# Optimization experiments

Hardware: AMD Instinct MI355X
Metric: run time of the kernel (lower is better)

Reference implementation:

```python
import jax, jax.numpy as jnp
import numpy as np

NEG = -1e9


def setup_inputs() -> dict:
    key = jax.random.key(0)
    ks = jax.random.split(key, 10)
    B, C, H, W = 4, 64, 64, 64
    Cq = C // 8
    x = jax.random.normal(ks[0], (B, C, H, W), dtype=jnp.float32)
    mask = jax.random.randint(ks[1], (B, 1, H, W), 0, 2, dtype=jnp.int32)
    # 1x1 conv params (out_ch, in_ch) + bias
    Wq = jax.random.normal(ks[2], (Cq, C), dtype=jnp.float32) * (1.0 / np.sqrt(C))
    bq = jnp.zeros((Cq,), dtype=jnp.float32)
    Wk = jax.random.normal(ks[3], (Cq, C), dtype=jnp.float32) * (1.0 / np.sqrt(C))
    bk = jnp.zeros((Cq,), dtype=jnp.float32)
    Wv = jax.random.normal(ks[4], (C, C), dtype=jnp.float32) * (1.0 / np.sqrt(C))
    bv = jnp.zeros((C,), dtype=jnp.float32)
    # torch inits gamma to 0; use small random so attention path contributes
    gamma = jax.random.normal(ks[5], (1,), dtype=jnp.float32) * 0.1
    return {"x": x, "mask": mask, "Wq": Wq, "bq": bq, "Wk": Wk, "bk": bk,
            "Wv": Wv, "bv": bv, "gamma": gamma}


def reference(x, mask, Wq, bq, Wk, bk, Wv, bv, gamma):
    B, C, H, W = x.shape
    N = H * W
    xf = x.reshape(B, C, N)                      # (B,C,N)
    # 1x1 convs == per-pixel linear projections
    q = jnp.einsum('oc,bcn->bno', Wq, xf) + bq   # (B,N,Cq)
    k = jnp.einsum('oc,bcn->bon', Wk, xf) + bk[None, :, None]  # (B,Cq,N)
    v = jnp.einsum('oc,bcn->bon', Wv, xf) + bv[None, :, None]  # (B,C,N)
    m = mask.reshape(B, N).astype(bool)
    logits = jnp.einsum('bno,bom->bnm', q, k)    # (B,N,N)
    valid = m[:, :, None] & m[:, None, :]        # outer-product validity mask
    logits = jnp.where(valid, logits, NEG)
    attn = jax.nn.softmax(logits, axis=-1)       # (B,N,N)
    out = jnp.einsum('bcj,bij->bci', v, attn)    # (B,C,N)
    out = out.reshape(B, C, H, W)
    return gamma * out + x
```

## Files before the change

### kernel.cpp

```cpp
#include <hip/hip_runtime.h>

typedef unsigned int uint;
typedef unsigned short ushort;
typedef __attribute__((ext_vector_type(8))) short short8;
typedef __attribute__((ext_vector_type(4))) float f32x4;
typedef __attribute__((ext_vector_type(16))) float f32x16;
typedef __attribute__((ext_vector_type(4))) uint uint4v;
typedef __attribute__((ext_vector_type(2))) uint uint2v;

#define BATCH 4
#define CH 64
#define NPIX 4096
#define LOG2E 1.44269504f

#define WSQ 0
#define WSK (BATCH * 128 * 512)
#define WSV (2 * BATCH * 128 * 512)

__device__ __forceinline__ ushort f2bf(float f) {
    union { float f; uint u; } a; a.f = f;
    const uint u = a.u;
    return (ushort)((u + 0x7FFFu + ((u >> 16) & 1u)) >> 16);
}
__device__ __forceinline__ uint pkbf(float a, float b) {
    return (uint)f2bf(a) | ((uint)f2bf(b) << 16);
}
__device__ __forceinline__ uint pkbf_fu(float a, float b) {
    union { float f; uint u; } x, y; x.f = a; y.f = b;
    return ((y.u + 0x8000u) & 0xFFFF0000u) | ((x.u + 0x8000u) >> 16);
}

__global__ __launch_bounds__(256) void proj_kernel(
    const float* __restrict__ x, const int* __restrict__ mask,
    const float* __restrict__ Wq, const float* __restrict__ bq,
    const float* __restrict__ Wk, const float* __restrict__ bk,
    const float* __restrict__ Wv, const float* __restrict__ bv,
    ushort* __restrict__ ws)
{
    __shared__ float wsh[16 * 64];
    __shared__ float bsh[16];
    const int g = blockIdx.y;
    const int tid = threadIdx.x;
    const int nout = (g == 0) ? 16 : 8;

    if (g == 0) {
        for (int i = tid; i < 512; i += 256) { wsh[i] = Wq[i]; wsh[512 + i] = Wk[i]; }
        if (tid < 8)  bsh[tid] = bq[tid];
        else if (tid < 16) bsh[tid] = bk[tid - 8];
    } else {
        const float* W = Wv + (g - 1) * 512;
        for (int i = tid; i < 512; i += 256) wsh[i] = W[i];
        if (tid < 8) bsh[tid] = bv[(g - 1) * 8 + tid];
    }
    __syncthreads();

    const int pix = blockIdx.x * 256 + tid;
    const int b = pix >> 12;
    const int n = pix & (NPIX - 1);
    const float* xb = x + (size_t)b * CH * NPIX + n;

    float acc[16];
#pragma unroll
    for (int o = 0; o < 16; o++) acc[o] = (o < nout) ? bsh[o] : 0.f;

#pragma unroll
    for (int c4 = 0; c4 < 16; c4++) {
        float xv0 = xb[(size_t)(c4 * 4 + 0) * NPIX];
        float xv1 = xb[(size_t)(c4 * 4 + 1) * NPIX];
        float xv2 = xb[(size_t)(c4 * 4 + 2) * NPIX];
        float xv3 = xb[(size_t)(c4 * 4 + 3) * NPIX];
        if (g == 0) {
#pragma unroll
            for (int o = 0; o < 16; o++) {
                const int base = (o < 8 ? 0 : 512) + (o & 7) * 64;
                float4 w = *(const float4*)&wsh[base + c4 * 4];
                acc[o] += w.x * xv0 + w.y * xv1 + w.z * xv2 + w.w * xv3;
            }
        } else {
#pragma unroll
            for (int o = 0; o < 8; o++) {
                float4 w = *(const float4*)&wsh[o * 64 + c4 * 4];
                acc[o] += w.x * xv0 + w.y * xv1 + w.z * xv2 + w.w * xv3;
            }
        }
    }

    const int jt = n >> 5, jl = n & 31;
    if (g == 0) {
        const int qm = mask[pix];
        {
            const float s = qm ? LOG2E : 0.f;
            uint4v lo, hi;
            lo.x = pkbf(acc[0] * s, acc[1] * s);
            lo.y = pkbf(acc[2] * s, acc[3] * s);
            lo.z = pkbf(acc[4] * s, acc[5] * s);
            lo.w = pkbf(acc[6] * s, acc[7] * s);
            hi.x = qm ? 0x3F80u : 0u;
            hi.y = 0u; hi.z = 0u; hi.w = 0u;
            ushort* qf = ws + WSQ + (size_t)b * 65536 + (size_t)jt * 512;
            *(uint4v*)(qf + jl * 8)       = lo;
            *(uint4v*)(qf + 256 + jl * 8) = hi;
        }
        {
            uint4v lo, hi;
            lo.x = pkbf(acc[8],  acc[9]);
            lo.y = pkbf(acc[10], acc[11]);
            lo.z = pkbf(acc[12], acc[13]);
            lo.w = pkbf(acc[14], acc[15]);
            hi.x = (uint)f2bf(qm ? 0.f : -1e30f);
            hi.y = 0u; hi.z = 0u; hi.w = 0u;
            ushort* kf = ws + WSK + (size_t)b * 65536 + (size_t)jt * 512;
            *(uint4v*)(kf + jl * 8)       = lo;
            *(uint4v*)(kf + 256 + jl * 8) = hi;
        }
    } else {
        const int h = jl >> 4, hp = (jl >> 3) & 1, jj = jl & 7;
        const int c0 = (g - 1) * 8;
        ushort* vt = ws + WSV + (size_t)b * 262144;
#pragma unroll
        for (int o = 0; o < 8; o++) {
            const int c = c0 + o, ct = c >> 5, cp = c & 31;
            vt[(size_t)((((jt * 2 + ct) * 2 + h) * 2 + hp) * 256) + cp * 8 + jj] = f2bf(acc[o]);
        }
    }
}

__global__ __launch_bounds__(512, 2) void attn_kernel(
    const ushort* __restrict__ ws, const float* __restrict__ x,
    const float* __restrict__ gamma, float* __restrict__ out)
{
    __shared__ float Obuf[8][32][36];
    __shared__ float Lb[2][8][32];
    __shared__ float Linv[2][32];

    const int tid  = threadIdx.x;
    const int wid  = tid >> 6;
    const int lane = tid & 63;
    const int hl   = lane >> 5;
    const int col  = lane & 31;
    const int b    = blockIdx.y;
    const int bx   = blockIdx.x;

    const ushort* qf = ws + WSQ + (size_t)b * 65536 + (size_t)(2 * bx) * 512;
    const ushort* kf = ws + WSK + (size_t)b * 65536;
    const ushort* vt = ws + WSV + (size_t)b * 262144;

    const short8 qfA = *(const short8*)(qf + lane * 8);
    const short8 qfB = *(const short8*)(qf + 512 + lane * 8);

    f32x16 accA0, accA1, accB0, accB1, zf;
#pragma unroll
    for (int r = 0; r < 16; r++) { accA0[r] = 0.f; accA1[r] = 0.f; accB0[r] = 0.f; accB1[r] = 0.f; zf[r] = 0.f; }
    float lsA = 0.f, lsB = 0.f;

    int jt = wid;
    uint4v kn   = *(const uint4v*)(kf + (size_t)jt * 512 + lane * 8);
    uint4v vn00 = *(const uint4v*)(vt + (size_t)((jt * 2 + 0) * 2 + 0) * 512 + lane * 8);
    uint4v vn01 = *(const uint4v*)(vt + (size_t)((jt * 2 + 0) * 2 + 1) * 512 + lane * 8);
    uint4v vn10 = *(const uint4v*)(vt + (size_t)((jt * 2 + 1) * 2 + 0) * 512 + lane * 8);
    uint4v vn11 = *(const uint4v*)(vt + (size_t)((jt * 2 + 1) * 2 + 1) * 512 + lane * 8);

#define QK_PV(SFRAG, LSUM, A0, A1) do {                                                              \
    float p[16];                                                                                     \
    _Pragma("unroll") for (int r = 0; r < 16; r++) p[r] = __builtin_amdgcn_exp2f((SFRAG)[r]);        \
    LSUM += (((p[0] + p[1]) + (p[2] + p[3])) + ((p[4] + p[5]) + (p[6] + p[7])))                      \
          + (((p[8] + p[9]) + (p[10] + p[11])) + ((p[12] + p[13]) + (p[14] + p[15])));               \
    uint P[8];                                                                                       \
    _Pragma("unroll") for (int r = 0; r < 8; r++) P[r] = pkbf_fu(p[2 * r], p[2 * r + 1]);            \
    const uint2v s02 = __builtin_amdgcn_permlane32_swap(P[0], P[2], false, false);                   \
    const uint2v s13 = __builtin_amdgcn_permlane32_swap(P[1], P[3], false, false);                   \
    const uint2v s46 = __builtin_amdgcn_permlane32_swap(P[4], P[6], false, false);                   \
    const uint2v s57 = __builtin_amdgcn_permlane32_swap(P[5], P[7], false, false);                   \
    uint4v B0, B1;                                                                                   \
    B0.x = s02.x; B0.y = s13.x; B0.z = s02.y; B0.w = s13.y;                                          \
    B1.x = s46.x; B1.y = s57.x; B1.z = s46.y; B1.w = s57.y;                                          \
    __builtin_amdgcn_s_setprio(1);                                                                   \
    A0 = __builtin_amdgcn_mfma_f32_32x32x16_bf16(*(const short8*)&c00, *(const short8*)&B0, A0, 0, 0, 0); \
    A0 = __builtin_amdgcn_mfma_f32_32x32x16_bf16(*(const short8*)&c01, *(const short8*)&B1, A0, 0, 0, 0); \
    A1 = __builtin_amdgcn_mfma_f32_32x32x16_bf16(*(const short8*)&c10, *(const short8*)&B0, A1, 0, 0, 0); \
    A1 = __builtin_amdgcn_mfma_f32_32x32x16_bf16(*(const short8*)&c11, *(const short8*)&B1, A1, 0, 0, 0); \
    __builtin_amdgcn_s_setprio(0);                                                                   \
} while (0)

    for (int t = 0; t < 16; t++) {
        const uint4v kc = kn, c00 = vn00, c01 = vn01, c10 = vn10, c11 = vn11;
        if (t < 15) {
            const int jn = jt + 8;
            kn   = *(const uint4v*)(kf + (size_t)jn * 512 + lane * 8);
            vn00 = *(const uint4v*)(vt + (size_t)((jn * 2 + 0) * 2 + 0) * 512 + lane * 8);
            vn01 = *(const uint4v*)(vt + (size_t)((jn * 2 + 0) * 2 + 1) * 512 + lane * 8);
            vn10 = *(const uint4v*)(vt + (size_t)((jn * 2 + 1) * 2 + 0) * 512 + lane * 8);
            vn11 = *(const uint4v*)(vt + (size_t)((jn * 2 + 1) * 2 + 1) * 512 + lane * 8);
        }

        const f32x16 sA = __builtin_amdgcn_mfma_f32_32x32x16_bf16(*(const short8*)&kc, qfA, zf, 0, 0, 0);
        const f32x16 sB = __builtin_amdgcn_mfma_f32_32x32x16_bf16(*(const short8*)&kc, qfB, zf, 0, 0, 0);

        QK_PV(sA, lsA, accA0, accA1);
        QK_PV(sB, lsB, accB0, accB1);

        jt += 8;
    }
#undef QK_PV

    const float lwA = lsA + __shfl_xor(lsA, 32);
    const float lwB = lsB + __shfl_xor(lsB, 32);
    if (hl == 0) { Lb[0][wid][col] = lwA; Lb[1][wid][col] = lwB; }
    __syncthreads();
    if (tid < 64) {
        const int q = tid >> 5, m = tid & 31;
        float s = 0.f;
#pragma unroll
        for (int w = 0; w < 8; w++) s += Lb[q][w][m];
        Linv[q][m] = 1.f / s;
    }

    const float gm = gamma[0];

#define MERGE_PASS(ACC, QSEL, CHALF) do {                                                            \
    __syncthreads();                                                                                 \
    _Pragma("unroll") for (int r = 0; r < 16; r++) {                                                 \
        const int crow = (r & 3) + 8 * (r >> 2) + 4 * hl;            \
        Obuf[wid][crow][col] = (ACC)[r];                                                             \
    }                                                                                                \
    __syncthreads();                                                                                 \
    {                                                                                                \
        const int c = tid >> 4, m0 = (tid & 15) * 2;                                                 \
        float o0 = 0.f, o1 = 0.f;                                                                    \
        _Pragma("unroll") for (int w = 0; w < 8; w++) { o0 += Obuf[w][c][m0]; o1 += Obuf[w][c][m0 + 1]; } \
        const size_t base = (((size_t)(b * CH + (CHALF) * 32 + c)) << 12) + bx * 64 + (QSEL) * 32 + m0; \
        const float2 xv = *(const float2*)&x[base];                                                  \
        float2 rv;                                                                                   \
        rv.x = gm * o0 * Linv[QSEL][m0]     + xv.x;                                                  \
        rv.y = gm * o1 * Linv[QSEL][m0 + 1] + xv.y;                                                  \
        *(float2*)&out[base] = rv;                                                                   \
    }                                                                                                \
} while (0)

    MERGE_PASS(accA0, 0, 0);
    MERGE_PASS(accA1, 0, 1);
    MERGE_PASS(accB0, 1, 0);
    MERGE_PASS(accB1, 1, 1);
#undef MERGE_PASS
}

extern "C" void kernel_launch(void* const* d_in, const int* in_sizes, int n_in,
                              void* d_out, int out_size, void* d_ws, size_t ws_size,
                              hipStream_t stream) {
    const float* x     = (const float*)d_in[0];
    const int*   mask  = (const int*)d_in[1];
    const float* Wq    = (const float*)d_in[2];
    const float* bq    = (const float*)d_in[3];
    const float* Wk    = (const float*)d_in[4];
    const float* bk    = (const float*)d_in[5];
    const float* Wv    = (const float*)d_in[6];
    const float* bv    = (const float*)d_in[7];
    const float* gamma = (const float*)d_in[8];
    float* out  = (float*)d_out;
    ushort* ws  = (ushort*)d_ws;

    proj_kernel<<<dim3(64, 9), 256, 0, stream>>>(x, mask, Wq, bq, Wk, bk, Wv, bv, ws);
    attn_kernel<<<dim3(64, 4), 512, 0, stream>>>(ws, x, gamma, out);
}
```

Baseline: 100.2 us.

## Compute softmax row sums via MFMA, use hardware bf16 pack, merge output passes

Moves the softmax denominator accumulation off the vector ALU by running extra MFMAs against a one-hot ones operand on the same bf16 P fragments. The software bf16 rounding is replaced with the v_cvt_pk_bf16_f32 instruction in both kernels. The epilogue is restructured to merge both channel halves per query block in one LDS pass with 128-bit loads and stores, halving the barrier rounds at the cost of doubling the LDS buffer. The row sums now come from bf16-rounded probabilities, which slightly changes numerics, and the extra MFMAs add matrix-unit work.

Measured after the change: 100.7 us. Within noise of the previous version (+0.5%).

```diff
diff --git a/kernel.cpp b/kernel.cpp
--- a/kernel.cpp
+++ b/kernel.cpp
@@ -22,12 +22,10 @@
     const uint u = a.u;
     return (ushort)((u + 0x7FFFu + ((u >> 16) & 1u)) >> 16);
 }
-__device__ __forceinline__ uint pkbf(float a, float b) {
-    return (uint)f2bf(a) | ((uint)f2bf(b) << 16);
-}
-__device__ __forceinline__ uint pkbf_fu(float a, float b) {
-    union { float f; uint u; } x, y; x.f = a; y.f = b;
-    return ((y.u + 0x8000u) & 0xFFFF0000u) | ((x.u + 0x8000u) >> 16);
+__device__ __forceinline__ uint cvtpk(float a, float b) {
+    uint r;
+    asm("v_cvt_pk_bf16_f32 %0, %1, %2" : "=v"(r) : "v"(a), "v"(b));
+    return r;
 }
 
 __global__ __launch_bounds__(256) void proj_kernel(
@@ -91,10 +89,10 @@
         {
             const float s = qm ? LOG2E : 0.f;
             uint4v lo, hi;
-            lo.x = pkbf(acc[0] * s, acc[1] * s);
-            lo.y = pkbf(acc[2] * s, acc[3] * s);
-            lo.z = pkbf(acc[4] * s, acc[5] * s);
-            lo.w = pkbf(acc[6] * s, acc[7] * s);
+            lo.x = cvtpk(acc[0] * s, acc[1] * s);
+            lo.y = cvtpk(acc[2] * s, acc[3] * s);
+            lo.z = cvtpk(acc[4] * s, acc[5] * s);
+            lo.w = cvtpk(acc[6] * s, acc[7] * s);
             hi.x = qm ? 0x3F80u : 0u;
             hi.y = 0u; hi.z = 0u; hi.w = 0u;
             ushort* qf = ws + WSQ + (size_t)b * 65536 + (size_t)jt * 512;
@@ -103,10 +101,10 @@
         }
         {
             uint4v lo, hi;
-            lo.x = pkbf(acc[8],  acc[9]);
-            lo.y = pkbf(acc[10], acc[11]);
-            lo.z = pkbf(acc[12], acc[13]);
-            lo.w = pkbf(acc[14], acc[15]);
+            lo.x = cvtpk(acc[8],  acc[9]);
+            lo.y = cvtpk(acc[10], acc[11]);
+            lo.z = cvtpk(acc[12], acc[13]);
+            lo.w = cvtpk(acc[14], acc[15]);
             hi.x = (uint)f2bf(qm ? 0.f : -1e30f);
             hi.y = 0u; hi.z = 0u; hi.w = 0u;
             ushort* kf = ws + WSK + (size_t)b * 65536 + (size_t)jt * 512;
@@ -129,7 +127,7 @@
     const ushort* __restrict__ ws, const float* __restrict__ x,
     const float* __restrict__ gamma, float* __restrict__ out)
 {
-    __shared__ float Obuf[8][32][36];
+    __shared__ float Obuf[8][64][36];
     __shared__ float Lb[2][8][32];
     __shared__ float Linv[2][32];
 
@@ -148,10 +146,19 @@
     const short8 qfA = *(const short8*)(qf + lane * 8);
     const short8 qfB = *(const short8*)(qf + 512 + lane * 8);
 
-    f32x16 accA0, accA1, accB0, accB1, zf;
-#pragma unroll
-    for (int r = 0; r < 16; r++) { accA0[r] = 0.f; accA1[r] = 0.f; accB0[r] = 0.f; accB1[r] = 0.f; zf[r] = 0.f; }
-    float lsA = 0.f, lsB = 0.f;
+    const uint ob = 0x3F803F80u;
+    uint4v oAv, oBv;
+    oAv.x = (col == 0) ? ob : 0u; oAv.y = oAv.x; oAv.z = oAv.x; oAv.w = oAv.x;
+    oBv.x = (col == 1) ? ob : 0u; oBv.y = oBv.x; oBv.z = oBv.x; oBv.w = oBv.x;
+    const short8 onesA = *(const short8*)&oAv;
+    const short8 onesB = *(const short8*)&oBv;
+
+    f32x16 accA0, accA1, accB0, accB1, accL, zf;
+#pragma unroll
+    for (int r = 0; r < 16; r++) {
+        accA0[r] = 0.f; accA1[r] = 0.f; accB0[r] = 0.f; accB1[r] = 0.f;
+        accL[r] = 0.f; zf[r] = 0.f;
+    }
 
     int jt = wid;
     uint4v kn   = *(const uint4v*)(kf + (size_t)jt * 512 + lane * 8);
@@ -160,13 +167,11 @@
     uint4v vn10 = *(const uint4v*)(vt + (size_t)((jt * 2 + 1) * 2 + 0) * 512 + lane * 8);
     uint4v vn11 = *(const uint4v*)(vt + (size_t)((jt * 2 + 1) * 2 + 1) * 512 + lane * 8);
 
-#define QK_PV(SFRAG, LSUM, A0, A1) do {                                                              \
+#define QK_PV(SFRAG, ONES, A0, A1) do {                                                              \
     float p[16];                                                                                     \
     _Pragma("unroll") for (int r = 0; r < 16; r++) p[r] = __builtin_amdgcn_exp2f((SFRAG)[r]);        \
-    LSUM += (((p[0] + p[1]) + (p[2] + p[3])) + ((p[4] + p[5]) + (p[6] + p[7])))                      \
-          + (((p[8] + p[9]) + (p[10] + p[11])) + ((p[12] + p[13]) + (p[14] + p[15])));               \
     uint P[8];                                                                                       \
-    _Pragma("unroll") for (int r = 0; r < 8; r++) P[r] = pkbf_fu(p[2 * r], p[2 * r + 1]);            \
+    _Pragma("unroll") for (int r = 0; r < 8; r++) P[r] = cvtpk(p[2 * r], p[2 * r + 1]);              \
     const uint2v s02 = __builtin_amdgcn_permlane32_swap(P[0], P[2], false, false);                   \
     const uint2v s13 = __builtin_amdgcn_permlane32_swap(P[1], P[3], false, false);                   \
     const uint2v s46 = __builtin_amdgcn_permlane32_swap(P[4], P[6], false, false);                   \
@@ -179,6 +184,8 @@
     A0 = __builtin_amdgcn_mfma_f32_32x32x16_bf16(*(const short8*)&c01, *(const short8*)&B1, A0, 0, 0, 0); \
     A1 = __builtin_amdgcn_mfma_f32_32x32x16_bf16(*(const short8*)&c10, *(const short8*)&B0, A1, 0, 0, 0); \
     A1 = __builtin_amdgcn_mfma_f32_32x32x16_bf16(*(const short8*)&c11, *(const short8*)&B1, A1, 0, 0, 0); \
+    accL = __builtin_amdgcn_mfma_f32_32x32x16_bf16(ONES, *(const short8*)&B0, accL, 0, 0, 0);        \
+    accL = __builtin_amdgcn_mfma_f32_32x32x16_bf16(ONES, *(const short8*)&B1, accL, 0, 0, 0);        \
     __builtin_amdgcn_s_setprio(0);                                                                   \
 } while (0)
 
@@ -196,16 +203,14 @@
         const f32x16 sA = __builtin_amdgcn_mfma_f32_32x32x16_bf16(*(const short8*)&kc, qfA, zf, 0, 0, 0);
         const f32x16 sB = __builtin_amdgcn_mfma_f32_32x32x16_bf16(*(const short8*)&kc, qfB, zf, 0, 0, 0);
 
-        QK_PV(sA, lsA, accA0, accA1);
-        QK_PV(sB, lsB, accB0, accB1);
+        QK_PV(sA, onesA, accA0, accA1);
+        QK_PV(sB, onesB, accB0, accB1);
 
         jt += 8;
     }
 #undef QK_PV
 
-    const float lwA = lsA + __shfl_xor(lsA, 32);
-    const float lwB = lsB + __shfl_xor(lsB, 32);
-    if (hl == 0) { Lb[0][wid][col] = lwA; Lb[1][wid][col] = lwB; }
+    if (hl == 0) { Lb[0][wid][col] = accL[0]; Lb[1][wid][col] = accL[1]; }
     __syncthreads();
     if (tid < 64) {
         const int q = tid >> 5, m = tid & 31;
@@ -217,30 +222,29 @@
 
     const float gm = gamma[0];
 
-#define MERGE_PASS(ACC, QSEL, CHALF) do {                                                            \
+#define MERGE_PASS(A0v, A1v, QSEL) do {                                                              \
     __syncthreads();                                                                                 \
     _Pragma("unroll") for (int r = 0; r < 16; r++) {                                                 \
         const int crow = (r & 3) + 8 * (r >> 2) + 4 * hl;            \
-        Obuf[wid][crow][col] = (ACC)[r];                                                             \
+        Obuf[wid][crow][col]      = (A0v)[r];                                                        \
+        Obuf[wid][32 + crow][col] = (A1v)[r];                                                        \
     }                                                                                                \
     __syncthreads();                                                                                 \
     {                                                                                                \
-        const int c = tid >> 4, m0 = (tid & 15) * 2;                                                 \
-        float o0 = 0.f, o1 = 0.f;                                                                    \
-        _Pragma("unroll") for (int w = 0; w < 8; w++) { o0 += Obuf[w][c][m0]; o1 += Obuf[w][c][m0 + 1]; } \
-        const size_t base = (((size_t)(b * CH + (CHALF) * 32 + c)) << 12) + bx * 64 + (QSEL) * 32 + m0; \
-        const float2 xv = *(const float2*)&x[base];                                                  \
-        float2 rv;                                                                                   \
-        rv.x = gm * o0 * Linv[QSEL][m0]     + xv.x;                                                  \
-        rv.y = gm * o1 * Linv[QSEL][m0 + 1] + xv.y;                                                  \
-        *(float2*)&out[base] = rv;                                                                   \
+        const int c = tid >> 3, m0 = (tid & 7) * 4;                                                  \
+        f32x4 o = {0.f, 0.f, 0.f, 0.f};                                                              \
+        _Pragma("unroll") for (int w = 0; w < 8; w++) o += *(const f32x4*)&Obuf[w][c][m0];            \
+        const size_t base = (((size_t)(b * CH + c)) << 12) + bx * 64 + (QSEL) * 32 + m0;             \
+        const f32x4 xv = *(const f32x4*)&x[base];                                                    \
+        f32x4 rv;                                                                                    \
+        _Pragma("unroll") for (int u = 0; u < 4; u++)                                                \
+            rv[u] = gm * o[u] * Linv[QSEL][m0 + u] + xv[u];                                          \
+        *(f32x4*)&out[base] = rv;                                                                    \
     }                                                                                                \
 } while (0)
 
-    MERGE_PASS(accA0, 0, 0);
-    MERGE_PASS(accA1, 0, 1);
-    MERGE_PASS(accB0, 1, 0);
-    MERGE_PASS(accB1, 1, 1);
+    MERGE_PASS(accA0, accA1, 0);
+    MERGE_PASS(accB0, accB1, 1);
 #undef MERGE_PASS
 }
 
```

## Compact valid keys per row group and skip masked key tiles in attention

Applied to the files above, without the earlier changes.

The projection kernel now stream-compacts each 256-pixel group's keys and values so valid (mask=1) keys come first, records per-group valid counts, stores per-pixel query masks, and computes per-channel V sums for the fully masked queries. The attention kernel builds a per-wave list of key tiles that contain valid keys and iterates only over those, skipping tiles that are entirely masked. Masked queries are given the uniform-attention result, the V mean, directly in the epilogue. Bf16 packing also switches to the hardware v_cvt_pk_bf16_f32 instruction. This adds preprocessing, extra workspace traffic and an indirect tile-index table, and it relies on masked keys contributing exp(-inf)=0, which matches the reference's -1e9 fill.

New measurement: 96.47 us. 1.04x faster.

```diff
diff --git a/kernel.cpp b/kernel.cpp
--- a/kernel.cpp
+++ b/kernel.cpp
@@ -2,6 +2,7 @@
 
 typedef unsigned int uint;
 typedef unsigned short ushort;
+typedef unsigned long long ull;
 typedef __attribute__((ext_vector_type(8))) short short8;
 typedef __attribute__((ext_vector_type(4))) float f32x4;
 typedef __attribute__((ext_vector_type(16))) float f32x16;
@@ -14,20 +15,21 @@
 #define LOG2E 1.44269504f
 
 #define WSQ 0
-#define WSK (BATCH * 128 * 512)
-#define WSV (2 * BATCH * 128 * 512)
+#define WSK 262144
+#define WSV 524288
+#define WSNV 1572864
+#define WSQM 1572928
+#define WSVPU 1589312
 
 __device__ __forceinline__ ushort f2bf(float f) {
     union { float f; uint u; } a; a.f = f;
     const uint u = a.u;
     return (ushort)((u + 0x7FFFu + ((u >> 16) & 1u)) >> 16);
 }
-__device__ __forceinline__ uint pkbf(float a, float b) {
-    return (uint)f2bf(a) | ((uint)f2bf(b) << 16);
-}
-__device__ __forceinline__ uint pkbf_fu(float a, float b) {
-    union { float f; uint u; } x, y; x.f = a; y.f = b;
-    return ((y.u + 0x8000u) & 0xFFFF0000u) | ((x.u + 0x8000u) >> 16);
+__device__ __forceinline__ uint cvtpk(float a, float b) {
+    uint r;
+    asm("v_cvt_pk_bf16_f32 %0, %1, %2" : "=v"(r) : "v"(a), "v"(b));
+    return r;
 }
 
 __global__ __launch_bounds__(256) void proj_kernel(
@@ -39,8 +41,11 @@
 {
     __shared__ float wsh[16 * 64];
     __shared__ float bsh[16];
+    __shared__ int   wcnt[4];
+    __shared__ float wvs[4][8];
     const int g = blockIdx.y;
     const int tid = threadIdx.x;
+    const int wid = tid >> 6, lane = tid & 63;
     const int nout = (g == 0) ? 16 : 8;
 
     if (g == 0) {
@@ -52,13 +57,16 @@
         for (int i = tid; i < 512; i += 256) wsh[i] = W[i];
         if (tid < 8) bsh[tid] = bv[(g - 1) * 8 + tid];
     }
-    __syncthreads();
 
     const int pix = blockIdx.x * 256 + tid;
     const int b = pix >> 12;
     const int n = pix & (NPIX - 1);
+    const int qm = mask[pix];
+    const ull bal = __ballot(qm != 0);
+    if (lane == 0) wcnt[wid] = __popcll(bal);
+    __syncthreads();
+
     const float* xb = x + (size_t)b * CH * NPIX + n;
-
     float acc[16];
 #pragma unroll
     for (int o = 0; o < 16; o++) acc[o] = (o < nout) ? bsh[o] : 0.f;
@@ -85,34 +93,48 @@
         }
     }
 
-    const int jt = n >> 5, jl = n & 31;
+    int offV = 0, offI = 0, nvb = 0;
+#pragma unroll
+    for (int w = 0; w < 4; w++) {
+        const int cw = wcnt[w];
+        if (w < wid) { offV += cw; offI += 64 - cw; }
+        nvb += cw;
+    }
+    const int rankV = __popcll(bal & ((1ull << lane) - 1ull));
+    const int slot = qm ? (offV + rankV) : (nvb + offI + (lane - rankV));
+    const int rr = n >> 8;
+    const int js = rr * 8 + (slot >> 5);
+    const int jl = slot & 31;
+
     if (g == 0) {
-        const int qm = mask[pix];
         {
+            const int jtq = n >> 5, jlq = n & 31;
             const float s = qm ? LOG2E : 0.f;
             uint4v lo, hi;
-            lo.x = pkbf(acc[0] * s, acc[1] * s);
-            lo.y = pkbf(acc[2] * s, acc[3] * s);
-            lo.z = pkbf(acc[4] * s, acc[5] * s);
-            lo.w = pkbf(acc[6] * s, acc[7] * s);
+            lo.x = cvtpk(acc[0] * s, acc[1] * s);
+            lo.y = cvtpk(acc[2] * s, acc[3] * s);
+            lo.z = cvtpk(acc[4] * s, acc[5] * s);
+            lo.w = cvtpk(acc[6] * s, acc[7] * s);
             hi.x = qm ? 0x3F80u : 0u;
             hi.y = 0u; hi.z = 0u; hi.w = 0u;
-            ushort* qf = ws + WSQ + (size_t)b * 65536 + (size_t)jt * 512;
-            *(uint4v*)(qf + jl * 8)       = lo;
-            *(uint4v*)(qf + 256 + jl * 8) = hi;
+            ushort* qf = ws + WSQ + (size_t)b * 65536 + (size_t)jtq * 512;
+            *(uint4v*)(qf + jlq * 8)       = lo;
+            *(uint4v*)(qf + 256 + jlq * 8) = hi;
         }
         {
             uint4v lo, hi;
-            lo.x = pkbf(acc[8],  acc[9]);
-            lo.y = pkbf(acc[10], acc[11]);
-            lo.z = pkbf(acc[12], acc[13]);
-            lo.w = pkbf(acc[14], acc[15]);
+            lo.x = cvtpk(acc[8],  acc[9]);
+            lo.y = cvtpk(acc[10], acc[11]);
+            lo.z = cvtpk(acc[12], acc[13]);
+            lo.w = cvtpk(acc[14], acc[15]);
             hi.x = (uint)f2bf(qm ? 0.f : -1e30f);
             hi.y = 0u; hi.z = 0u; hi.w = 0u;
-            ushort* kf = ws + WSK + (size_t)b * 65536 + (size_t)jt * 512;
+            ushort* kf = ws + WSK + (size_t)b * 65536 + (size_t)js * 512;
             *(uint4v*)(kf + jl * 8)       = lo;
             *(uint4v*)(kf + 256 + jl * 8) = hi;
         }
+        if (tid == 0) ws[WSNV + b * 16 + rr] = (ushort)nvb;
+        ws[WSQM + pix] = (ushort)qm;
     } else {
         const int h = jl >> 4, hp = (jl >> 3) & 1, jj = jl & 7;
         const int c0 = (g - 1) * 8;
@@ -120,7 +142,20 @@
 #pragma unroll
         for (int o = 0; o < 8; o++) {
             const int c = c0 + o, ct = c >> 5, cp = c & 31;
-            vt[(size_t)((((jt * 2 + ct) * 2 + h) * 2 + hp) * 256) + cp * 8 + jj] = f2bf(acc[o]);
+            vt[(size_t)((((js * 2 + ct) * 2 + h) * 2 + hp) * 256) + cp * 8 + jj] = f2bf(acc[o]);
+        }
+#pragma unroll
+        for (int o = 0; o < 8; o++) {
+            float v = acc[o];
+#pragma unroll
+            for (int off = 32; off; off >>= 1) v += __shfl_down(v, off);
+            if (lane == 0) wvs[wid][o] = v;
+        }
+        __syncthreads();
+        if (tid < 8) {
+            const float t = wvs[0][tid] + wvs[1][tid] + wvs[2][tid] + wvs[3][tid];
+            float* vpf = (float*)(ws + WSVPU);
+            vpf[(b * 64 + c0 + tid) * 16 + (blockIdx.x & 15)] = t;
         }
     }
 }
@@ -132,6 +167,10 @@
     __shared__ float Obuf[8][32][36];
     __shared__ float Lb[2][8][32];
     __shared__ float Linv[2][32];
+    __shared__ float VmeanS[64];
+    __shared__ ushort qmS[64];
+    __shared__ ushort nvS[16];
+    __shared__ ushort jtT[8][17];
 
     const int tid  = threadIdx.x;
     const int wid  = tid >> 6;
@@ -148,17 +187,51 @@
     const short8 qfA = *(const short8*)(qf + lane * 8);
     const short8 qfB = *(const short8*)(qf + 512 + lane * 8);
 
+    if (tid < 16) nvS[tid] = ws[WSNV + b * 16 + tid];
+    if (tid >= 64 && tid < 128) qmS[tid - 64] = ws[WSQM + b * 4096 + bx * 64 + (tid - 64)];
+    if (tid >= 128 && tid < 192) {
+        const int c = tid - 128;
+        const float* vpf = (const float*)(ws + WSVPU);
+        float s = 0.f;
+#pragma unroll
+        for (int k2 = 0; k2 < 16; k2++) s += vpf[(b * 64 + c) * 16 + k2];
+        VmeanS[c] = s * (1.0f / 4096.0f);
+    }
+    __syncthreads();
+
+    int A = 0;
+#pragma unroll
+    for (int r2 = 0; r2 < 16; r2++) {
+        int a = ((int)nvS[r2] + 31) >> 5; if (a > 8) a = 8;
+        A += a;
+    }
+    if (tid < 128) {
+        const int w = tid >> 4, ii = tid & 15, ci = w + ii * 8;
+        int Acc = 0, ent = 0;
+#pragma unroll
+        for (int r2 = 0; r2 < 16; r2++) {
+            int a = ((int)nvS[r2] + 31) >> 5; if (a > 8) a = 8;
+            if (ci >= Acc && ci < Acc + a) ent = r2 * 8 + (ci - Acc);
+            Acc += a;
+        }
+        jtT[w][ii] = (ushort)ent;
+    }
+    if (tid < 8) jtT[tid][16] = 0;
+    __syncthreads();
+
+    const int niter = (A - wid + 7) >> 3;
+
     f32x16 accA0, accA1, accB0, accB1, zf;
 #pragma unroll
     for (int r = 0; r < 16; r++) { accA0[r] = 0.f; accA1[r] = 0.f; accB0[r] = 0.f; accB1[r] = 0.f; zf[r] = 0.f; }
     float lsA = 0.f, lsB = 0.f;
 
-    int jt = wid;
-    uint4v kn   = *(const uint4v*)(kf + (size_t)jt * 512 + lane * 8);
-    uint4v vn00 = *(const uint4v*)(vt + (size_t)((jt * 2 + 0) * 2 + 0) * 512 + lane * 8);
-    uint4v vn01 = *(const uint4v*)(vt + (size_t)((jt * 2 + 0) * 2 + 1) * 512 + lane * 8);
-    uint4v vn10 = *(const uint4v*)(vt + (size_t)((jt * 2 + 1) * 2 + 0) * 512 + lane * 8);
-    uint4v vn11 = *(const uint4v*)(vt + (size_t)((jt * 2 + 1) * 2 + 1) * 512 + lane * 8);
+    int jc = jtT[wid][0];
+    uint4v kn   = *(const uint4v*)(kf + (size_t)jc * 512 + lane * 8);
+    uint4v vn00 = *(const uint4v*)(vt + (size_t)((jc * 2 + 0) * 2 + 0) * 512 + lane * 8);
+    uint4v vn01 = *(const uint4v*)(vt + (size_t)((jc * 2 + 0) * 2 + 1) * 512 + lane * 8);
+    uint4v vn10 = *(const uint4v*)(vt + (size_t)((jc * 2 + 1) * 2 + 0) * 512 + lane * 8);
+    uint4v vn11 = *(const uint4v*)(vt + (size_t)((jc * 2 + 1) * 2 + 1) * 512 + lane * 8);
 
 #define QK_PV(SFRAG, LSUM, A0, A1) do {                                                              \
     float p[16];                                                                                     \
@@ -166,7 +239,7 @@
     LSUM += (((p[0] + p[1]) + (p[2] + p[3])) + ((p[4] + p[5]) + (p[6] + p[7])))                      \
           + (((p[8] + p[9]) + (p[10] + p[11])) + ((p[12] + p[13]) + (p[14] + p[15])));               \
     uint P[8];                                                                                       \
-    _Pragma("unroll") for (int r = 0; r < 8; r++) P[r] = pkbf_fu(p[2 * r], p[2 * r + 1]);            \
+    _Pragma("unroll") for (int r = 0; r < 8; r++) P[r] = cvtpk(p[2 * r], p[2 * r + 1]);              \
     const uint2v s02 = __builtin_amdgcn_permlane32_swap(P[0], P[2], false, false);                   \
     const uint2v s13 = __builtin_amdgcn_permlane32_swap(P[1], P[3], false, false);                   \
     const uint2v s46 = __builtin_amdgcn_permlane32_swap(P[4], P[6], false, false);                   \
@@ -182,10 +255,10 @@
     __builtin_amdgcn_s_setprio(0);                                                                   \
 } while (0)
 
-    for (int t = 0; t < 16; t++) {
+    for (int i = 0; i < niter; i++) {
+        const int jn = jtT[wid][i + 1];
         const uint4v kc = kn, c00 = vn00, c01 = vn01, c10 = vn10, c11 = vn11;
-        if (t < 15) {
-            const int jn = jt + 8;
+        if (i + 1 < niter) {
             kn   = *(const uint4v*)(kf + (size_t)jn * 512 + lane * 8);
             vn00 = *(const uint4v*)(vt + (size_t)((jn * 2 + 0) * 2 + 0) * 512 + lane * 8);
             vn01 = *(const uint4v*)(vt + (size_t)((jn * 2 + 0) * 2 + 1) * 512 + lane * 8);
@@ -198,8 +271,6 @@
 
         QK_PV(sA, lsA, accA0, accA1);
         QK_PV(sB, lsB, accB0, accB1);
-
-        jt += 8;
     }
 #undef QK_PV
 
@@ -228,11 +299,13 @@
         const int c = tid >> 4, m0 = (tid & 15) * 2;                                                 \
         float o0 = 0.f, o1 = 0.f;                                                                    \
         _Pragma("unroll") for (int w = 0; w < 8; w++) { o0 += Obuf[w][c][m0]; o1 += Obuf[w][c][m0 + 1]; } \
-        const size_t base = (((size_t)(b * CH + (CHALF) * 32 + c)) << 12) + bx * 64 + (QSEL) * 32 + m0; \
+        const int cg = (CHALF) * 32 + c;                                                             \
+        const int mi = (QSEL) * 32 + m0;                                                             \
+        const size_t base = (((size_t)(b * CH + cg)) << 12) + bx * 64 + (QSEL) * 32 + m0;            \
         const float2 xv = *(const float2*)&x[base];                                                  \
         float2 rv;                                                                                   \
-        rv.x = gm * o0 * Linv[QSEL][m0]     + xv.x;                                                  \
-        rv.y = gm * o1 * Linv[QSEL][m0 + 1] + xv.y;                                                  \
+        rv.x = (qmS[mi]     ? gm * o0 * Linv[QSEL][m0]     : gm * VmeanS[cg]) + xv.x;                \
+        rv.y = (qmS[mi + 1] ? gm * o1 * Linv[QSEL][m0 + 1] : gm * VmeanS[cg]) + xv.y;                \
         *(float2*)&out[base] = rv;                                                                   \
     }                                                                                                \
 } while (0)
```
